# Performance work log

Measured on AMD Instinct MI355X. Metric: run time of the kernel, lower is better.

## Reference

```python
import jax, jax.numpy as jnp
import numpy as np
import math

B, H, S, D = 4, 16, 2048, 64  # batch, heads, seq, head dim
HEAD_NUM = 64                 # V value dim == Linear in_features
OUT_DIM = 64                  # input4_dim
SCALE = math.sqrt(D)          # scale_factor = sqrt(input3_dim)


def setup_inputs() -> dict:
    key = jax.random.key(0)
    k1, k2, k3, k4, k5 = jax.random.split(key, 5)
    return {
        "q": jax.random.normal(k1, (B, H, S, D), dtype=jnp.float32),
        "k": jax.random.normal(k2, (B, H, S, D), dtype=jnp.float32),
        "v": jax.random.normal(k3, (B, H, S, HEAD_NUM), dtype=jnp.float32),
        "w_out": jax.random.normal(k4, (OUT_DIM, HEAD_NUM), dtype=jnp.float32) * 0.05,
        "b_out": jax.random.normal(k5, (OUT_DIM,), dtype=jnp.float32) * 0.05,
    }


def reference(q, k, v, w_out, b_out):
    # scores = Q K^T / sqrt(d)   -> [B, H, S, S]
    scores = jnp.einsum("bhqd,bhkd->bhqk", q, k) / jnp.float32(SCALE)
    attn = jax.nn.softmax(scores, axis=-1)
    # dropout is identity (eval / p=0)
    y = jnp.einsum("bhqk,bhke->bhqe", attn, v)  # [B, H, S, HEAD_NUM]
    out = jnp.einsum("bhqe,oe->bhqo", y, w_out) + b_out
    return out
```

## Files before the change

### kernel.cpp

```cpp
#include <hip/hip_runtime.h>
#include <math.h>

typedef __attribute__((ext_vector_type(8))) short bf16x8;
typedef __attribute__((ext_vector_type(4))) float f32x4;
typedef __attribute__((ext_vector_type(16))) float f32x16;

#define S_LEN 2048
#define DH 64
#define NHEAD 64
#define HEAD_ELEMS (S_LEN * DH)
#define NT (S_LEN / 64)

static __device__ __forceinline__ unsigned short f2bf(float f) {
  union { float f; unsigned u; } v; v.f = f;
  return (unsigned short)((v.u + 0x7fffu + ((v.u >> 16) & 1u)) >> 16);
}

__global__ __launch_bounds__(256)
void prep(const float* __restrict__ k, const float* __restrict__ v,
          unsigned short* __restrict__ ko, unsigned short* __restrict__ vt) {
  __shared__ float t[64][65];
  const int tid = threadIdx.x;
  if (blockIdx.x < 2048) {
    const int head = blockIdx.x >> 5;
    const int kt   = blockIdx.x & 31;
    const float* kp = k + (size_t)head * HEAD_ELEMS;
    unsigned short* kout = ko + (size_t)head * HEAD_ELEMS + (size_t)kt * 4096;
    #pragma unroll
    for (int i = 0; i < 2; ++i) {
      const int c     = i * 256 + tid;
      const int chunk = c >> 6;
      const int tt    = chunk >> 2;
      const int d     = chunk & 3;
      const int l     = c & 63;
      const int row   = kt * 64 + tt * 32 + (l & 31);
      const int col   = d * 16 + (l >> 5) * 8;
      const float* src = kp + (size_t)row * DH + col;
      float4 a = *(const float4*)src;
      float4 b = *(const float4*)(src + 4);
      bf16x8 r;
      r[0]=(short)f2bf(a.x); r[1]=(short)f2bf(a.y); r[2]=(short)f2bf(a.z); r[3]=(short)f2bf(a.w);
      r[4]=(short)f2bf(b.x); r[5]=(short)f2bf(b.y); r[6]=(short)f2bf(b.z); r[7]=(short)f2bf(b.w);
      *(bf16x8*)(kout + (size_t)chunk * 512 + l * 8) = r;
    }
  } else {
    const int bi   = blockIdx.x - 2048;
    const int head = bi >> 5;
    const int kc   = bi & 31;
    const float* vp = v + (size_t)head * HEAD_ELEMS + (size_t)kc * 64 * DH;
    #pragma unroll
    for (int i = 0; i < 4; ++i) {
      int fi = tid + i * 256;
      int kk = fi >> 4, e4 = (fi & 15) * 4;
      float4 f = *(const float4*)(vp + kk * DH + e4);
      t[kk][e4] = f.x; t[kk][e4+1] = f.y; t[kk][e4+2] = f.z; t[kk][e4+3] = f.w;
    }
    __syncthreads();
    unsigned short* vout = vt + (size_t)head * HEAD_ELEMS + (size_t)kc * 4096;
    #pragma unroll
    for (int i = 0; i < 2; ++i) {
      const int c     = i * 256 + tid;
      const int chunk = c >> 6;
      const int t2    = chunk >> 2;
      const int kh    = (chunk >> 1) & 1;
      const int eh    = chunk & 1;
      const int l     = c & 63;
      const int e     = eh * 32 + (l & 31);
      const int kr    = t2 * 32 + kh * 16 + (l >> 5) * 8;
      bf16x8 r;
      #pragma unroll
      for (int j = 0; j < 8; ++j) r[j] = (short)f2bf(t[kr + j][e]);
      *(bf16x8*)(vout + (size_t)chunk * 512 + l * 8) = r;
    }
  }
}

__global__ __launch_bounds__(256, 4)
void attn_reg(const float* __restrict__ qg, const unsigned short* __restrict__ kfb,
              const unsigned short* __restrict__ vfb, const float* __restrict__ wg,
              const float* __restrict__ bg, float* __restrict__ og) {
  __shared__ __align__(16) unsigned short Ylds[4][2048];
  __shared__ float stats[4][32];

  const int tid = threadIdx.x;
  const int w   = tid >> 6;
  const int l   = tid & 63;
  const int lq  = l & 31;
  const int hi  = l >> 5;

  const int bxs  = ((blockIdx.x & 7) << 7) | (blockIdx.x >> 3);
  const int bh   = bxs >> 4;
  const int qblk = bxs & 15;

  const unsigned short* kh_ = kfb + (size_t)bh * HEAD_ELEMS + l * 8;
  const unsigned short* vh_ = vfb + (size_t)bh * HEAD_ELEMS + l * 8;

  bf16x8 qf[4];
  {
    const float QS = 0.125f * 1.44269504f;
    const float* qfp = qg + (size_t)bh * HEAD_ELEMS
                     + (size_t)(qblk * 128 + w * 32 + lq) * DH + hi * 8;
    #pragma unroll
    for (int d = 0; d < 4; ++d) {
      float4 f0 = *(const float4*)(qfp + d * 16);
      float4 f1 = *(const float4*)(qfp + d * 16 + 4);
      bf16x8 a;
      a[0]=(short)f2bf(f0.x*QS); a[1]=(short)f2bf(f0.y*QS);
      a[2]=(short)f2bf(f0.z*QS); a[3]=(short)f2bf(f0.w*QS);
      a[4]=(short)f2bf(f1.x*QS); a[5]=(short)f2bf(f1.y*QS);
      a[6]=(short)f2bf(f1.z*QS); a[7]=(short)f2bf(f1.w*QS);
      qf[d] = a;
    }
  }

  f32x16 yacc0, yacc1, zv;
  #pragma unroll
  for (int i = 0; i < 16; ++i) { yacc0[i] = 0.f; yacc1[i] = 0.f; zv[i] = 0.f; }
  float lsum = 0.f;

  for (int kt = 0; kt < NT; ++kt) {
    #pragma unroll
    for (int t = 0; t < 2; ++t) {
      const unsigned short* kp = kh_ + (size_t)(kt * 8 + t * 4) * 512;
      const unsigned short* vp = vh_ + (size_t)(kt * 8 + t * 4) * 512;
      bf16x8 kf0 = *(const bf16x8*)(kp);
      bf16x8 kf1 = *(const bf16x8*)(kp + 512);
      bf16x8 kf2 = *(const bf16x8*)(kp + 1024);
      bf16x8 kf3 = *(const bf16x8*)(kp + 1536);
      bf16x8 v00 = *(const bf16x8*)(vp);
      bf16x8 v10 = *(const bf16x8*)(vp + 512);
      bf16x8 v01 = *(const bf16x8*)(vp + 1024);
      bf16x8 v11 = *(const bf16x8*)(vp + 1536);

      f32x16 s;
      __builtin_amdgcn_s_setprio(1);
      s = __builtin_amdgcn_mfma_f32_32x32x16_bf16(kf0, qf[0], zv, 0, 0, 0);
      s = __builtin_amdgcn_mfma_f32_32x32x16_bf16(kf1, qf[1], s, 0, 0, 0);
      s = __builtin_amdgcn_mfma_f32_32x32x16_bf16(kf2, qf[2], s, 0, 0, 0);
      s = __builtin_amdgcn_mfma_f32_32x32x16_bf16(kf3, qf[3], s, 0, 0, 0);
      __builtin_amdgcn_s_setprio(0);

      unsigned pk[8];
      #pragma unroll
      for (int i = 0; i < 8; ++i) {
        float a = exp2f(s[2 * i]);
        float b = exp2f(s[2 * i + 1]);
        lsum += a + b;
        asm("v_cvt_pk_bf16_f32 %0, %1, %2" : "=v"(pk[i]) : "v"(a), "v"(b));
      }
      asm volatile("v_permlane32_swap_b32 %0, %1" : "+v"(pk[0]), "+v"(pk[2]));
      asm volatile("v_permlane32_swap_b32 %0, %1" : "+v"(pk[1]), "+v"(pk[3]));
      asm volatile("v_permlane32_swap_b32 %0, %1" : "+v"(pk[4]), "+v"(pk[6]));
      asm volatile("v_permlane32_swap_b32 %0, %1" : "+v"(pk[5]), "+v"(pk[7]));
      union { unsigned u[4]; bf16x8 v; } f0, f1;
      f0.u[0] = pk[0]; f0.u[1] = pk[1]; f0.u[2] = pk[2]; f0.u[3] = pk[3];
      f1.u[0] = pk[4]; f1.u[1] = pk[5]; f1.u[2] = pk[6]; f1.u[3] = pk[7];

      __builtin_amdgcn_s_setprio(1);
      yacc0 = __builtin_amdgcn_mfma_f32_32x32x16_bf16(f0.v, v00, yacc0, 0, 0, 0);
      yacc0 = __builtin_amdgcn_mfma_f32_32x32x16_bf16(f1.v, v01, yacc0, 0, 0, 0);
      yacc1 = __builtin_amdgcn_mfma_f32_32x32x16_bf16(f0.v, v10, yacc1, 0, 0, 0);
      yacc1 = __builtin_amdgcn_mfma_f32_32x32x16_bf16(f1.v, v11, yacc1, 0, 0, 0);
      __builtin_amdgcn_s_setprio(0);
    }
  }

  lsum += __shfl_xor(lsum, 32);
  if (hi == 0) stats[w][lq] = 1.0f / lsum;
  asm volatile("s_waitcnt lgkmcnt(0)" ::: "memory");
  __builtin_amdgcn_sched_barrier(0);

  {
    char* Y = (char*)Ylds[w];
    #pragma unroll
    for (int et = 0; et < 2; ++et) {
      f32x16& ya = et ? yacc1 : yacc0;
      const int e = et * 32 + lq;
      #pragma unroll
      for (int r = 0; r < 16; ++r) {
        const int qr_ = (r & 3) + 8 * (r >> 2) + 4 * hi;
        *(unsigned short*)(Y + qr_ * 128 + (((e >> 3) ^ (qr_ & 7)) << 4) + (e & 7) * 2)
            = f2bf(ya[r] * stats[w][qr_]);
      }
    }
  }
  asm volatile("s_waitcnt lgkmcnt(0)" ::: "memory");
  __builtin_amdgcn_sched_barrier(0);

  f32x16 o0, o1;
  #pragma unroll
  for (int i = 0; i < 16; ++i) { o0[i] = 0.f; o1[i] = 0.f; }
  {
    const char* Y = (const char*)Ylds[w];
    #pragma unroll
    for (int es = 0; es < 4; ++es) {
      bf16x8 ya = *(const bf16x8*)(Y + lq * 128 + (((es * 2 + hi) ^ (lq & 7)) << 4));
      #pragma unroll
      for (int ot = 0; ot < 2; ++ot) {
        const float* wp = wg + (size_t)(ot * 32 + lq) * 64 + es * 16 + hi * 8;
        float4 w0 = *(const float4*)wp;
        float4 w1 = *(const float4*)(wp + 4);
        bf16x8 wf;
        wf[0]=(short)f2bf(w0.x); wf[1]=(short)f2bf(w0.y); wf[2]=(short)f2bf(w0.z); wf[3]=(short)f2bf(w0.w);
        wf[4]=(short)f2bf(w1.x); wf[5]=(short)f2bf(w1.y); wf[6]=(short)f2bf(w1.z); wf[7]=(short)f2bf(w1.w);
        if (ot == 0) o0 = __builtin_amdgcn_mfma_f32_32x32x16_bf16(ya, wf, o0, 0, 0, 0);
        else         o1 = __builtin_amdgcn_mfma_f32_32x32x16_bf16(ya, wf, o1, 0, 0, 0);
      }
    }
  }
  const float b0 = bg[lq], b1 = bg[32 + lq];
  float* orow = og + (size_t)bh * HEAD_ELEMS + (size_t)(qblk * 128 + w * 32) * DH;
  #pragma unroll
  for (int r = 0; r < 16; ++r) {
    const int qr_ = (r & 3) + 8 * (r >> 2) + 4 * hi;
    orow[qr_ * 64 + lq]      = o0[r] + b0;
    orow[qr_ * 64 + 32 + lq] = o1[r] + b1;
  }
}

static __device__ __forceinline__ int swz(int row, int col) {
  return row * 128 + ((((col >> 3) ^ (row & 7))) << 4) + ((col & 7) << 1);
}

__global__ __launch_bounds__(256, 2)
void attn_proj_kernel(const float* __restrict__ qg, const float* __restrict__ kg,
                      const float* __restrict__ vg, const float* __restrict__ wg,
                      const float* __restrict__ bg, float* __restrict__ og) {
  __shared__ unsigned short lK[64 * 64];
  __shared__ unsigned short lV[64 * 64];
  __shared__ unsigned short lP[4][16 * 64];

  const int tid  = threadIdx.x;
  const int wave = tid >> 6;
  const int lane = tid & 63;
  const int lg   = lane >> 4;
  const int lr   = lane & 15;
  const int bh = blockIdx.x >> 5;
  const int qt = blockIdx.x & 31;
  const size_t head_off = (size_t)bh * S_LEN * 64;
  const float* qp = qg + head_off;
  const float* kp = kg + head_off;
  const float* vp = vg + head_off;

  const int qrow = qt * 64 + wave * 16 + lr;
  bf16x8 qa[2];
  {
    const float* qr = qp + (size_t)qrow * 64 + lg * 8;
    #pragma unroll
    for (int s = 0; s < 2; ++s) {
      float4 f0 = *(const float4*)(qr + s * 32);
      float4 f1 = *(const float4*)(qr + s * 32 + 4);
      bf16x8 a;
      a[0]=(short)f2bf(f0.x*0.125f); a[1]=(short)f2bf(f0.y*0.125f);
      a[2]=(short)f2bf(f0.z*0.125f); a[3]=(short)f2bf(f0.w*0.125f);
      a[4]=(short)f2bf(f1.x*0.125f); a[5]=(short)f2bf(f1.y*0.125f);
      a[6]=(short)f2bf(f1.z*0.125f); a[7]=(short)f2bf(f1.w*0.125f);
      qa[s] = a;
    }
  }
  f32x4 yacc[4];
  #pragma unroll
  for (int e = 0; e < 4; ++e) yacc[e] = (f32x4){0.f, 0.f, 0.f, 0.f};
  float mrow[4], lrow[4];
  #pragma unroll
  for (int r = 0; r < 4; ++r) { mrow[r] = -INFINITY; lrow[r] = 0.f; }

  for (int kt = 0; kt < S_LEN / 64; ++kt) {
    __syncthreads();
    #pragma unroll
    for (int i = 0; i < 4; ++i) {
      int n = tid + i * 256;
      int row = n >> 4;
      int c4 = (n & 15) * 4;
      const size_t goff = (size_t)(kt * 64 + row) * 64 + c4;
      float4 kf = *(const float4*)(kp + goff);
      unsigned p0 = (unsigned)f2bf(kf.x) | ((unsigned)f2bf(kf.y) << 16);
      unsigned p1 = (unsigned)f2bf(kf.z) | ((unsigned)f2bf(kf.w) << 16);
      uint2 pk2; pk2.x = p0; pk2.y = p1;
      *(uint2*)((char*)lK + swz(row, c4)) = pk2;
      float4 vf = *(const float4*)(vp + goff);
      *(unsigned short*)((char*)lV + swz(c4 + 0, row)) = f2bf(vf.x);
      *(unsigned short*)((char*)lV + swz(c4 + 1, row)) = f2bf(vf.y);
      *(unsigned short*)((char*)lV + swz(c4 + 2, row)) = f2bf(vf.z);
      *(unsigned short*)((char*)lV + swz(c4 + 3, row)) = f2bf(vf.w);
    }
    __syncthreads();
    f32x4 sacc[4];
    #pragma unroll
    for (int c = 0; c < 4; ++c) {
      sacc[c] = (f32x4){0.f, 0.f, 0.f, 0.f};
      #pragma unroll
      for (int s = 0; s < 2; ++s) {
        bf16x8 kb2 = *(const bf16x8*)((const char*)lK + swz(c * 16 + lr, s * 32 + lg * 8));
        sacc[c] = __builtin_amdgcn_mfma_f32_16x16x32_bf16(qa[s], kb2, sacc[c], 0, 0, 0);
      }
    }
    float mt[4], alpha[4];
    #pragma unroll
    for (int r = 0; r < 4; ++r) {
      float mm = fmaxf(fmaxf(sacc[0][r], sacc[1][r]), fmaxf(sacc[2][r], sacc[3][r]));
      mm = fmaxf(mm, __shfl_xor(mm, 1));
      mm = fmaxf(mm, __shfl_xor(mm, 2));
      mm = fmaxf(mm, __shfl_xor(mm, 4));
      mm = fmaxf(mm, __shfl_xor(mm, 8));
      mt[r] = fmaxf(mrow[r], mm);
      alpha[r] = __expf(mrow[r] - mt[r]);
      mrow[r] = mt[r];
    }
    #pragma unroll
    for (int c = 0; c < 4; ++c)
      #pragma unroll
      for (int r = 0; r < 4; ++r) sacc[c][r] = __expf(sacc[c][r] - mt[r]);
    #pragma unroll
    for (int r = 0; r < 4; ++r) {
      float sum = sacc[0][r] + sacc[1][r] + sacc[2][r] + sacc[3][r];
      sum += __shfl_xor(sum, 1);
      sum += __shfl_xor(sum, 2);
      sum += __shfl_xor(sum, 4);
      sum += __shfl_xor(sum, 8);
      lrow[r] = lrow[r] * alpha[r] + sum;
      #pragma unroll
      for (int e = 0; e < 4; ++e) yacc[e][r] *= alpha[r];
    }
    unsigned short* pw = lP[wave];
    #pragma unroll
    for (int c = 0; c < 4; ++c)
      #pragma unroll
      for (int r = 0; r < 4; ++r)
        *(unsigned short*)((char*)pw + swz(lg * 4 + r, c * 16 + lr)) = f2bf(sacc[c][r]);
    asm volatile("s_waitcnt lgkmcnt(0)" ::: "memory");
    #pragma unroll
    for (int s = 0; s < 2; ++s) {
      bf16x8 pa = *(const bf16x8*)((const char*)pw + swz(lr, s * 32 + lg * 8));
      #pragma unroll
      for (int e = 0; e < 4; ++e) {
        bf16x8 vb = *(const bf16x8*)((const char*)lV + swz(e * 16 + lr, s * 32 + lg * 8));
        yacc[e] = __builtin_amdgcn_mfma_f32_16x16x32_bf16(pa, vb, yacc[e], 0, 0, 0);
      }
    }
  }
  unsigned short* pw = lP[wave];
  #pragma unroll
  for (int e = 0; e < 4; ++e)
    #pragma unroll
    for (int r = 0; r < 4; ++r)
      *(unsigned short*)((char*)pw + swz(lg * 4 + r, e * 16 + lr)) = f2bf(yacc[e][r] / lrow[r]);
  asm volatile("s_waitcnt lgkmcnt(0)" ::: "memory");
  f32x4 oacc[4];
  #pragma unroll
  for (int c = 0; c < 4; ++c) oacc[c] = (f32x4){0.f, 0.f, 0.f, 0.f};
  #pragma unroll
  for (int s = 0; s < 2; ++s) {
    bf16x8 ya = *(const bf16x8*)((const char*)pw + swz(lr, s * 32 + lg * 8));
    #pragma unroll
    for (int c = 0; c < 4; ++c) {
      const float* wp = wg + (size_t)(c * 16 + lr) * 64 + s * 32 + lg * 8;
      float4 f0 = *(const float4*)wp;
      float4 f1 = *(const float4*)(wp + 4);
      bf16x8 wb;
      wb[0]=(short)f2bf(f0.x); wb[1]=(short)f2bf(f0.y); wb[2]=(short)f2bf(f0.z); wb[3]=(short)f2bf(f0.w);
      wb[4]=(short)f2bf(f1.x); wb[5]=(short)f2bf(f1.y); wb[6]=(short)f2bf(f1.z); wb[7]=(short)f2bf(f1.w);
      oacc[c] = __builtin_amdgcn_mfma_f32_16x16x32_bf16(ya, wb, oacc[c], 0, 0, 0);
    }
  }
  float* op = og + head_off + (size_t)(qt * 64 + wave * 16) * 64;
  #pragma unroll
  for (int c = 0; c < 4; ++c) {
    float bias = bg[c * 16 + lr];
    #pragma unroll
    for (int r = 0; r < 4; ++r)
      op[(size_t)(lg * 4 + r) * 64 + c * 16 + lr] = oacc[c][r] + bias;
  }
}

extern "C" void kernel_launch(void* const* d_in, const int* in_sizes, int n_in,
                              void* d_out, int out_size, void* d_ws, size_t ws_size,
                              hipStream_t stream) {
  const float* q = (const float*)d_in[0];
  const float* k = (const float*)d_in[1];
  const float* v = (const float*)d_in[2];
  const float* w = (const float*)d_in[3];
  const float* b = (const float*)d_in[4];
  float* out = (float*)d_out;

  const size_t tensor_elems = (size_t)NHEAD * HEAD_ELEMS;
  const size_t need = 2ull * tensor_elems * sizeof(unsigned short);

  if (ws_size >= need) {
    unsigned short* kws = (unsigned short*)d_ws;
    unsigned short* vws = kws + tensor_elems;
    prep<<<4096, 256, 0, stream>>>(k, v, kws, vws);
    attn_reg<<<1024, 256, 0, stream>>>(q, kws, vws, w, b, out);
  } else {
    attn_proj_kernel<<<64 * 32, 256, 0, stream>>>(q, k, v, w, b, out);
  }
}
```

Before: 236.7 us.

## Double-buffer K/V register loads in attention loop and split row-sum accumulators

Restructures the main key loop into a software-pipelined form with two register buffers, so the K/V fragments for the next 32-key step are loaded from global memory before the current step's MFMAs and softmax run. The row-sum is split into two accumulators to shorten the dependent add chain. The extra live registers push the launch bound occupancy hint from 4 to 3 blocks per CU, trading fewer resident waves for more in-flight loads per wave.

```diff
diff --git a/kernel.cpp b/kernel.cpp
--- a/kernel.cpp
+++ b/kernel.cpp
@@ -75,7 +75,47 @@
   }
 }
 
-__global__ __launch_bounds__(256, 4)
+#define LOADKV(KB, VB, it) do {                                              \
+    const unsigned short* kp_ = kh_ + (size_t)(it) * 2048;                   \
+    const unsigned short* vp_ = vh_ + (size_t)(it) * 2048;                   \
+    KB[0] = *(const bf16x8*)(kp_);        KB[1] = *(const bf16x8*)(kp_ + 512);  \
+    KB[2] = *(const bf16x8*)(kp_ + 1024); KB[3] = *(const bf16x8*)(kp_ + 1536); \
+    VB[0] = *(const bf16x8*)(vp_);        VB[1] = *(const bf16x8*)(vp_ + 512);  \
+    VB[2] = *(const bf16x8*)(vp_ + 1024); VB[3] = *(const bf16x8*)(vp_ + 1536); \
+  } while (0)
+
+#define COMPUTE(KB, VB) do {                                                 \
+    f32x16 s;                                                                \
+    __builtin_amdgcn_s_setprio(1);                                           \
+    s = __builtin_amdgcn_mfma_f32_32x32x16_bf16(KB[0], qf[0], zv, 0, 0, 0);  \
+    s = __builtin_amdgcn_mfma_f32_32x32x16_bf16(KB[1], qf[1], s, 0, 0, 0);   \
+    s = __builtin_amdgcn_mfma_f32_32x32x16_bf16(KB[2], qf[2], s, 0, 0, 0);   \
+    s = __builtin_amdgcn_mfma_f32_32x32x16_bf16(KB[3], qf[3], s, 0, 0, 0);   \
+    __builtin_amdgcn_s_setprio(0);                                           \
+    unsigned pk[8];                                                          \
+    _Pragma("unroll")                                                        \
+    for (int i_ = 0; i_ < 8; ++i_) {                                         \
+      float ea = exp2f(s[2 * i_]);                                           \
+      float eb = exp2f(s[2 * i_ + 1]);                                       \
+      if (i_ & 1) ls1 += ea + eb; else ls0 += ea + eb;                       \
+      asm("v_cvt_pk_bf16_f32 %0, %1, %2" : "=v"(pk[i_]) : "v"(ea), "v"(eb)); \
+    }                                                                        \
+    asm volatile("v_permlane32_swap_b32 %0, %1" : "+v"(pk[0]), "+v"(pk[2])); \
+    asm volatile("v_permlane32_swap_b32 %0, %1" : "+v"(pk[1]), "+v"(pk[3])); \
+    asm volatile("v_permlane32_swap_b32 %0, %1" : "+v"(pk[4]), "+v"(pk[6])); \
+    asm volatile("v_permlane32_swap_b32 %0, %1" : "+v"(pk[5]), "+v"(pk[7])); \
+    union { unsigned u[4]; bf16x8 v; } pf0, pf1;                             \
+    pf0.u[0] = pk[0]; pf0.u[1] = pk[1]; pf0.u[2] = pk[2]; pf0.u[3] = pk[3];  \
+    pf1.u[0] = pk[4]; pf1.u[1] = pk[5]; pf1.u[2] = pk[6]; pf1.u[3] = pk[7];  \
+    __builtin_amdgcn_s_setprio(1);                                           \
+    yacc0 = __builtin_amdgcn_mfma_f32_32x32x16_bf16(pf0.v, VB[0], yacc0, 0, 0, 0); \
+    yacc0 = __builtin_amdgcn_mfma_f32_32x32x16_bf16(pf1.v, VB[2], yacc0, 0, 0, 0); \
+    yacc1 = __builtin_amdgcn_mfma_f32_32x32x16_bf16(pf0.v, VB[1], yacc1, 0, 0, 0); \
+    yacc1 = __builtin_amdgcn_mfma_f32_32x32x16_bf16(pf1.v, VB[3], yacc1, 0, 0, 0); \
+    __builtin_amdgcn_s_setprio(0);                                           \
+  } while (0)
+
+__global__ __launch_bounds__(256, 3)
 void attn_reg(const float* __restrict__ qg, const unsigned short* __restrict__ kfb,
               const unsigned short* __restrict__ vfb, const float* __restrict__ wg,
               const float* __restrict__ bg, float* __restrict__ og) {
@@ -116,54 +156,17 @@
   f32x16 yacc0, yacc1, zv;
   #pragma unroll
   for (int i = 0; i < 16; ++i) { yacc0[i] = 0.f; yacc1[i] = 0.f; zv[i] = 0.f; }
-  float lsum = 0.f;
-
-  for (int kt = 0; kt < NT; ++kt) {
-    #pragma unroll
-    for (int t = 0; t < 2; ++t) {
-      const unsigned short* kp = kh_ + (size_t)(kt * 8 + t * 4) * 512;
-      const unsigned short* vp = vh_ + (size_t)(kt * 8 + t * 4) * 512;
-      bf16x8 kf0 = *(const bf16x8*)(kp);
-      bf16x8 kf1 = *(const bf16x8*)(kp + 512);
-      bf16x8 kf2 = *(const bf16x8*)(kp + 1024);
-      bf16x8 kf3 = *(const bf16x8*)(kp + 1536);
-      bf16x8 v00 = *(const bf16x8*)(vp);
-      bf16x8 v10 = *(const bf16x8*)(vp + 512);
-      bf16x8 v01 = *(const bf16x8*)(vp + 1024);
-      bf16x8 v11 = *(const bf16x8*)(vp + 1536);
-
-      f32x16 s;
-      __builtin_amdgcn_s_setprio(1);
-      s = __builtin_amdgcn_mfma_f32_32x32x16_bf16(kf0, qf[0], zv, 0, 0, 0);
-      s = __builtin_amdgcn_mfma_f32_32x32x16_bf16(kf1, qf[1], s, 0, 0, 0);
-      s = __builtin_amdgcn_mfma_f32_32x32x16_bf16(kf2, qf[2], s, 0, 0, 0);
-      s = __builtin_amdgcn_mfma_f32_32x32x16_bf16(kf3, qf[3], s, 0, 0, 0);
-      __builtin_amdgcn_s_setprio(0);
-
-      unsigned pk[8];
-      #pragma unroll
-      for (int i = 0; i < 8; ++i) {
-        float a = exp2f(s[2 * i]);
-        float b = exp2f(s[2 * i + 1]);
-        lsum += a + b;
-        asm("v_cvt_pk_bf16_f32 %0, %1, %2" : "=v"(pk[i]) : "v"(a), "v"(b));
-      }
-      asm volatile("v_permlane32_swap_b32 %0, %1" : "+v"(pk[0]), "+v"(pk[2]));
-      asm volatile("v_permlane32_swap_b32 %0, %1" : "+v"(pk[1]), "+v"(pk[3]));
-      asm volatile("v_permlane32_swap_b32 %0, %1" : "+v"(pk[4]), "+v"(pk[6]));
-      asm volatile("v_permlane32_swap_b32 %0, %1" : "+v"(pk[5]), "+v"(pk[7]));
-      union { unsigned u[4]; bf16x8 v; } f0, f1;
-      f0.u[0] = pk[0]; f0.u[1] = pk[1]; f0.u[2] = pk[2]; f0.u[3] = pk[3];
-      f1.u[0] = pk[4]; f1.u[1] = pk[5]; f1.u[2] = pk[6]; f1.u[3] = pk[7];
-
-      __builtin_amdgcn_s_setprio(1);
-      yacc0 = __builtin_amdgcn_mfma_f32_32x32x16_bf16(f0.v, v00, yacc0, 0, 0, 0);
-      yacc0 = __builtin_amdgcn_mfma_f32_32x32x16_bf16(f1.v, v01, yacc0, 0, 0, 0);
-      yacc1 = __builtin_amdgcn_mfma_f32_32x32x16_bf16(f0.v, v10, yacc1, 0, 0, 0);
-      yacc1 = __builtin_amdgcn_mfma_f32_32x32x16_bf16(f1.v, v11, yacc1, 0, 0, 0);
-      __builtin_amdgcn_s_setprio(0);
-    }
-  }
+  float ls0 = 0.f, ls1 = 0.f;
+
+  bf16x8 kA[4], vA[4], kB[4], vB[4];
+  LOADKV(kA, vA, 0);
+  for (int it = 0; it < 2 * NT; it += 2) {
+    LOADKV(kB, vB, it + 1);
+    COMPUTE(kA, vA);
+    if (it + 2 < 2 * NT) LOADKV(kA, vA, it + 2);
+    COMPUTE(kB, vB);
+  }
+  float lsum = ls0 + ls1;
 
   lsum += __shfl_xor(lsum, 32);
   if (hi == 0) stats[w][lq] = 1.0f / lsum;
```

Result: faster. 231.0 us (-2.4%).

## Process two query tiles per wave to reuse K/V fragment loads

Applied to the files above, without the earlier changes.

Each wave now handles two 32-row query tiles (256 queries per block, 512 blocks) and shares every K and V fragment load across both tiles, with interleaved QK MFMAs for the two tiles. The aim is to halve global/L2 K/V traffic per query and give the scheduler independent MFMA chains to overlap with exp work. The cost is roughly doubled accumulator registers, occupancy bounds lowered from 4 to 2 blocks, and half as many blocks to fill the GPU.

```diff
diff --git a/kernel.cpp b/kernel.cpp
--- a/kernel.cpp
+++ b/kernel.cpp
@@ -75,12 +75,82 @@
   }
 }
 
-__global__ __launch_bounds__(256, 4)
-void attn_reg(const float* __restrict__ qg, const unsigned short* __restrict__ kfb,
-              const unsigned short* __restrict__ vfb, const float* __restrict__ wg,
-              const float* __restrict__ bg, float* __restrict__ og) {
+#define SOFTMAX_PV(S, LS, Y0, Y1) do {                                        \
+    unsigned pk[8];                                                           \
+    _Pragma("unroll")                                                         \
+    for (int i_ = 0; i_ < 8; ++i_) {                                          \
+      float ea = exp2f(S[2 * i_]);                                            \
+      float eb = exp2f(S[2 * i_ + 1]);                                        \
+      LS += ea + eb;                                                          \
+      asm("v_cvt_pk_bf16_f32 %0, %1, %2" : "=v"(pk[i_]) : "v"(ea), "v"(eb));  \
+    }                                                                         \
+    asm volatile("v_permlane32_swap_b32 %0, %1" : "+v"(pk[0]), "+v"(pk[2]));  \
+    asm volatile("v_permlane32_swap_b32 %0, %1" : "+v"(pk[1]), "+v"(pk[3]));  \
+    asm volatile("v_permlane32_swap_b32 %0, %1" : "+v"(pk[4]), "+v"(pk[6]));  \
+    asm volatile("v_permlane32_swap_b32 %0, %1" : "+v"(pk[5]), "+v"(pk[7]));  \
+    union { unsigned u[4]; bf16x8 v; } pf0, pf1;                              \
+    pf0.u[0] = pk[0]; pf0.u[1] = pk[1]; pf0.u[2] = pk[2]; pf0.u[3] = pk[3];   \
+    pf1.u[0] = pk[4]; pf1.u[1] = pk[5]; pf1.u[2] = pk[6]; pf1.u[3] = pk[7];   \
+    __builtin_amdgcn_s_setprio(1);                                            \
+    Y0 = __builtin_amdgcn_mfma_f32_32x32x16_bf16(pf0.v, vf[0], Y0, 0, 0, 0);  \
+    Y0 = __builtin_amdgcn_mfma_f32_32x32x16_bf16(pf1.v, vf[2], Y0, 0, 0, 0);  \
+    Y1 = __builtin_amdgcn_mfma_f32_32x32x16_bf16(pf0.v, vf[1], Y1, 0, 0, 0);  \
+    Y1 = __builtin_amdgcn_mfma_f32_32x32x16_bf16(pf1.v, vf[3], Y1, 0, 0, 0);  \
+    __builtin_amdgcn_s_setprio(0);                                            \
+  } while (0)
+
+#define EPILOGUE(Y0, Y1, T2) do {                                             \
+    char* Y = (char*)Ylds[w];                                                 \
+    _Pragma("unroll")                                                         \
+    for (int et = 0; et < 2; ++et) {                                          \
+      f32x16& ya = et ? Y1 : Y0;                                              \
+      const int e = et * 32 + lq;                                             \
+      _Pragma("unroll")                                                       \
+      for (int r = 0; r < 16; ++r) {                                          \
+        const int qr_ = (r & 3) + 8 * (r >> 2) + 4 * hi;                      \
+        *(unsigned short*)(Y + qr_ * 128 + (((e >> 3) ^ (qr_ & 7)) << 4) + (e & 7) * 2) \
+            = f2bf(ya[r] * stats[w][(T2) * 32 + qr_]);                        \
+      }                                                                       \
+    }                                                                         \
+    asm volatile("s_waitcnt lgkmcnt(0)" ::: "memory");                        \
+    __builtin_amdgcn_sched_barrier(0);                                        \
+    f32x16 o0, o1;                                                            \
+    _Pragma("unroll")                                                         \
+    for (int i = 0; i < 16; ++i) { o0[i] = 0.f; o1[i] = 0.f; }                \
+    _Pragma("unroll")                                                         \
+    for (int es = 0; es < 4; ++es) {                                          \
+      bf16x8 ya = *(const bf16x8*)((const char*)Ylds[w] + lq * 128 + (((es * 2 + hi) ^ (lq & 7)) << 4)); \
+      _Pragma("unroll")                                                       \
+      for (int ot = 0; ot < 2; ++ot) {                                        \
+        const float* wp = wg + (size_t)(ot * 32 + lq) * 64 + es * 16 + hi * 8; \
+        float4 w0 = *(const float4*)wp;                                       \
+        float4 w1 = *(const float4*)(wp + 4);                                 \
+        bf16x8 wf;                                                            \
+        wf[0]=(short)f2bf(w0.x); wf[1]=(short)f2bf(w0.y); wf[2]=(short)f2bf(w0.z); wf[3]=(short)f2bf(w0.w); \
+        wf[4]=(short)f2bf(w1.x); wf[5]=(short)f2bf(w1.y); wf[6]=(short)f2bf(w1.z); wf[7]=(short)f2bf(w1.w); \
+        if (ot == 0) o0 = __builtin_amdgcn_mfma_f32_32x32x16_bf16(ya, wf, o0, 0, 0, 0); \
+        else         o1 = __builtin_amdgcn_mfma_f32_32x32x16_bf16(ya, wf, o1, 0, 0, 0); \
+      }                                                                       \
+    }                                                                         \
+    const float b0 = bg[lq], b1 = bg[32 + lq];                                \
+    float* orow = og + (size_t)bh * HEAD_ELEMS                                \
+                + (size_t)(qblk * 256 + (T2) * 128 + w * 32) * DH;            \
+    _Pragma("unroll")                                                         \
+    for (int r = 0; r < 16; ++r) {                                            \
+      const int qr_ = (r & 3) + 8 * (r >> 2) + 4 * hi;                        \
+      orow[qr_ * 64 + lq]      = o0[r] + b0;                                  \
+      orow[qr_ * 64 + 32 + lq] = o1[r] + b1;                                  \
+    }                                                                         \
+    asm volatile("s_waitcnt lgkmcnt(0)" ::: "memory");                        \
+    __builtin_amdgcn_sched_barrier(0);                                        \
+  } while (0)
+
+__global__ __launch_bounds__(256, 2)
+void attn_reg2(const float* __restrict__ qg, const unsigned short* __restrict__ kfb,
+               const unsigned short* __restrict__ vfb, const float* __restrict__ wg,
+               const float* __restrict__ bg, float* __restrict__ og) {
   __shared__ __align__(16) unsigned short Ylds[4][2048];
-  __shared__ float stats[4][32];
+  __shared__ float stats[4][64];
 
   const int tid = threadIdx.x;
   const int w   = tid >> 6;
@@ -88,134 +158,72 @@
   const int lq  = l & 31;
   const int hi  = l >> 5;
 
-  const int bxs  = ((blockIdx.x & 7) << 7) | (blockIdx.x >> 3);
-  const int bh   = bxs >> 4;
-  const int qblk = bxs & 15;
+  const int bxs  = ((blockIdx.x & 7) << 6) | (blockIdx.x >> 3);
+  const int bh   = bxs >> 3;
+  const int qblk = bxs & 7;
 
   const unsigned short* kh_ = kfb + (size_t)bh * HEAD_ELEMS + l * 8;
   const unsigned short* vh_ = vfb + (size_t)bh * HEAD_ELEMS + l * 8;
 
-  bf16x8 qf[4];
+  bf16x8 qa[4], qb[4];
   {
     const float QS = 0.125f * 1.44269504f;
-    const float* qfp = qg + (size_t)bh * HEAD_ELEMS
-                     + (size_t)(qblk * 128 + w * 32 + lq) * DH + hi * 8;
-    #pragma unroll
-    for (int d = 0; d < 4; ++d) {
-      float4 f0 = *(const float4*)(qfp + d * 16);
-      float4 f1 = *(const float4*)(qfp + d * 16 + 4);
-      bf16x8 a;
-      a[0]=(short)f2bf(f0.x*QS); a[1]=(short)f2bf(f0.y*QS);
-      a[2]=(short)f2bf(f0.z*QS); a[3]=(short)f2bf(f0.w*QS);
-      a[4]=(short)f2bf(f1.x*QS); a[5]=(short)f2bf(f1.y*QS);
-      a[6]=(short)f2bf(f1.z*QS); a[7]=(short)f2bf(f1.w*QS);
-      qf[d] = a;
-    }
-  }
-
-  f32x16 yacc0, yacc1, zv;
-  #pragma unroll
-  for (int i = 0; i < 16; ++i) { yacc0[i] = 0.f; yacc1[i] = 0.f; zv[i] = 0.f; }
-  float lsum = 0.f;
-
-  for (int kt = 0; kt < NT; ++kt) {
-    #pragma unroll
-    for (int t = 0; t < 2; ++t) {
-      const unsigned short* kp = kh_ + (size_t)(kt * 8 + t * 4) * 512;
-      const unsigned short* vp = vh_ + (size_t)(kt * 8 + t * 4) * 512;
-      bf16x8 kf0 = *(const bf16x8*)(kp);
-      bf16x8 kf1 = *(const bf16x8*)(kp + 512);
-      bf16x8 kf2 = *(const bf16x8*)(kp + 1024);
-      bf16x8 kf3 = *(const bf16x8*)(kp + 1536);
-      bf16x8 v00 = *(const bf16x8*)(vp);
-      bf16x8 v10 = *(const bf16x8*)(vp + 512);
-      bf16x8 v01 = *(const bf16x8*)(vp + 1024);
-      bf16x8 v11 = *(const bf16x8*)(vp + 1536);
-
-      f32x16 s;
-      __builtin_amdgcn_s_setprio(1);
-      s = __builtin_amdgcn_mfma_f32_32x32x16_bf16(kf0, qf[0], zv, 0, 0, 0);
-      s = __builtin_amdgcn_mfma_f32_32x32x16_bf16(kf1, qf[1], s, 0, 0, 0);
-      s = __builtin_amdgcn_mfma_f32_32x32x16_bf16(kf2, qf[2], s, 0, 0, 0);
-      s = __builtin_amdgcn_mfma_f32_32x32x16_bf16(kf3, qf[3], s, 0, 0, 0);
-      __builtin_amdgcn_s_setprio(0);
-
-      unsigned pk[8];
-      #pragma unroll
-      for (int i = 0; i < 8; ++i) {
-        float a = exp2f(s[2 * i]);
-        float b = exp2f(s[2 * i + 1]);
-        lsum += a + b;
-        asm("v_cvt_pk_bf16_f32 %0, %1, %2" : "=v"(pk[i]) : "v"(a), "v"(b));
+    #pragma unroll
+    for (int t2 = 0; t2 < 2; ++t2) {
+      const float* qfp = qg + (size_t)bh * HEAD_ELEMS
+                       + (size_t)(qblk * 256 + t2 * 128 + w * 32 + lq) * DH + hi * 8;
+      #pragma unroll
+      for (int d = 0; d < 4; ++d) {
+        float4 f0 = *(const float4*)(qfp + d * 16);
+        float4 f1 = *(const float4*)(qfp + d * 16 + 4);
+        bf16x8 a;
+        a[0]=(short)f2bf(f0.x*QS); a[1]=(short)f2bf(f0.y*QS);
+        a[2]=(short)f2bf(f0.z*QS); a[3]=(short)f2bf(f0.w*QS);
+        a[4]=(short)f2bf(f1.x*QS); a[5]=(short)f2bf(f1.y*QS);
+        a[6]=(short)f2bf(f1.z*QS); a[7]=(short)f2bf(f1.w*QS);
+        if (t2 == 0) qa[d] = a; else qb[d] = a;
       }
-      asm volatile("v_permlane32_swap_b32 %0, %1" : "+v"(pk[0]), "+v"(pk[2]));
-      asm volatile("v_permlane32_swap_b32 %0, %1" : "+v"(pk[1]), "+v"(pk[3]));
-      asm volatile("v_permlane32_swap_b32 %0, %1" : "+v"(pk[4]), "+v"(pk[6]));
-      asm volatile("v_permlane32_swap_b32 %0, %1" : "+v"(pk[5]), "+v"(pk[7]));
-      union { unsigned u[4]; bf16x8 v; } f0, f1;
-      f0.u[0] = pk[0]; f0.u[1] = pk[1]; f0.u[2] = pk[2]; f0.u[3] = pk[3];
-      f1.u[0] = pk[4]; f1.u[1] = pk[5]; f1.u[2] = pk[6]; f1.u[3] = pk[7];
-
-      __builtin_amdgcn_s_setprio(1);
-      yacc0 = __builtin_amdgcn_mfma_f32_32x32x16_bf16(f0.v, v00, yacc0, 0, 0, 0);
-      yacc0 = __builtin_amdgcn_mfma_f32_32x32x16_bf16(f1.v, v01, yacc0, 0, 0, 0);
-      yacc1 = __builtin_amdgcn_mfma_f32_32x32x16_bf16(f0.v, v10, yacc1, 0, 0, 0);
-      yacc1 = __builtin_amdgcn_mfma_f32_32x32x16_bf16(f1.v, v11, yacc1, 0, 0, 0);
-      __builtin_amdgcn_s_setprio(0);
-    }
-  }
-
-  lsum += __shfl_xor(lsum, 32);
-  if (hi == 0) stats[w][lq] = 1.0f / lsum;
+    }
+  }
+
+  f32x16 ya0, ya1, yb0, yb1, zv;
+  #pragma unroll
+  for (int i = 0; i < 16; ++i) { ya0[i]=0.f; ya1[i]=0.f; yb0[i]=0.f; yb1[i]=0.f; zv[i]=0.f; }
+  float lsA = 0.f, lsB = 0.f;
+
+  for (int it = 0; it < 2 * NT; ++it) {
+    const unsigned short* kp_ = kh_ + (size_t)it * 2048;
+    const unsigned short* vp_ = vh_ + (size_t)it * 2048;
+    bf16x8 kf[4], vf[4];
+    kf[0] = *(const bf16x8*)(kp_);        kf[1] = *(const bf16x8*)(kp_ + 512);
+    kf[2] = *(const bf16x8*)(kp_ + 1024); kf[3] = *(const bf16x8*)(kp_ + 1536);
+    vf[0] = *(const bf16x8*)(vp_);        vf[1] = *(const bf16x8*)(vp_ + 512);
+    vf[2] = *(const bf16x8*)(vp_ + 1024); vf[3] = *(const bf16x8*)(vp_ + 1536);
+
+    f32x16 sA, sB;
+    __builtin_amdgcn_s_setprio(1);
+    sA = __builtin_amdgcn_mfma_f32_32x32x16_bf16(kf[0], qa[0], zv, 0, 0, 0);
+    sB = __builtin_amdgcn_mfma_f32_32x32x16_bf16(kf[0], qb[0], zv, 0, 0, 0);
+    sA = __builtin_amdgcn_mfma_f32_32x32x16_bf16(kf[1], qa[1], sA, 0, 0, 0);
+    sB = __builtin_amdgcn_mfma_f32_32x32x16_bf16(kf[1], qb[1], sB, 0, 0, 0);
+    sA = __builtin_amdgcn_mfma_f32_32x32x16_bf16(kf[2], qa[2], sA, 0, 0, 0);
+    sB = __builtin_amdgcn_mfma_f32_32x32x16_bf16(kf[2], qb[2], sB, 0, 0, 0);
+    sA = __builtin_amdgcn_mfma_f32_32x32x16_bf16(kf[3], qa[3], sA, 0, 0, 0);
+    sB = __builtin_amdgcn_mfma_f32_32x32x16_bf16(kf[3], qb[3], sB, 0, 0, 0);
+    __builtin_amdgcn_s_setprio(0);
+
+    SOFTMAX_PV(sA, lsA, ya0, ya1);
+    SOFTMAX_PV(sB, lsB, yb0, yb1);
+  }
+
+  lsA += __shfl_xor(lsA, 32);
+  lsB += __shfl_xor(lsB, 32);
+  if (hi == 0) { stats[w][lq] = 1.0f / lsA; stats[w][32 + lq] = 1.0f / lsB; }
   asm volatile("s_waitcnt lgkmcnt(0)" ::: "memory");
   __builtin_amdgcn_sched_barrier(0);
 
-  {
-    char* Y = (char*)Ylds[w];
-    #pragma unroll
-    for (int et = 0; et < 2; ++et) {
-      f32x16& ya = et ? yacc1 : yacc0;
-      const int e = et * 32 + lq;
-      #pragma unroll
-      for (int r = 0; r < 16; ++r) {
-        const int qr_ = (r & 3) + 8 * (r >> 2) + 4 * hi;
-        *(unsigned short*)(Y + qr_ * 128 + (((e >> 3) ^ (qr_ & 7)) << 4) + (e & 7) * 2)
-            = f2bf(ya[r] * stats[w][qr_]);
-      }
-    }
-  }
-  asm volatile("s_waitcnt lgkmcnt(0)" ::: "memory");
-  __builtin_amdgcn_sched_barrier(0);
-
-  f32x16 o0, o1;
-  #pragma unroll
-  for (int i = 0; i < 16; ++i) { o0[i] = 0.f; o1[i] = 0.f; }
-  {
-    const char* Y = (const char*)Ylds[w];
-    #pragma unroll
-    for (int es = 0; es < 4; ++es) {
-      bf16x8 ya = *(const bf16x8*)(Y + lq * 128 + (((es * 2 + hi) ^ (lq & 7)) << 4));
-      #pragma unroll
-      for (int ot = 0; ot < 2; ++ot) {
-        const float* wp = wg + (size_t)(ot * 32 + lq) * 64 + es * 16 + hi * 8;
-        float4 w0 = *(const float4*)wp;
-        float4 w1 = *(const float4*)(wp + 4);
-        bf16x8 wf;
-        wf[0]=(short)f2bf(w0.x); wf[1]=(short)f2bf(w0.y); wf[2]=(short)f2bf(w0.z); wf[3]=(short)f2bf(w0.w);
-        wf[4]=(short)f2bf(w1.x); wf[5]=(short)f2bf(w1.y); wf[6]=(short)f2bf(w1.z); wf[7]=(short)f2bf(w1.w);
-        if (ot == 0) o0 = __builtin_amdgcn_mfma_f32_32x32x16_bf16(ya, wf, o0, 0, 0, 0);
-        else         o1 = __builtin_amdgcn_mfma_f32_32x32x16_bf16(ya, wf, o1, 0, 0, 0);
-      }
-    }
-  }
-  const float b0 = bg[lq], b1 = bg[32 + lq];
-  float* orow = og + (size_t)bh * HEAD_ELEMS + (size_t)(qblk * 128 + w * 32) * DH;
-  #pragma unroll
-  for (int r = 0; r < 16; ++r) {
-    const int qr_ = (r & 3) + 8 * (r >> 2) + 4 * hi;
-    orow[qr_ * 64 + lq]      = o0[r] + b0;
-    orow[qr_ * 64 + 32 + lq] = o1[r] + b1;
-  }
+  EPILOGUE(ya0, ya1, 0);
+  EPILOGUE(yb0, yb1, 1);
 }
 
 static __device__ __forceinline__ int swz(int row, int col) {
@@ -390,7 +398,7 @@
     unsigned short* kws = (unsigned short*)d_ws;
     unsigned short* vws = kws + tensor_elems;
     prep<<<4096, 256, 0, stream>>>(k, v, kws, vws);
-    attn_reg<<<1024, 256, 0, stream>>>(q, kws, vws, w, b, out);
+    attn_reg2<<<512, 256, 0, stream>>>(q, kws, vws, w, b, out);
   } else {
     attn_proj_kernel<<<64 * 32, 256, 0, stream>>>(q, k, v, w, b, out);
   }
```

Result: faster. 229.6 us (-3.0%).
